# Kernel optimization log

Measured on AMD Instinct MI355X. Metric: run time of the kernel, lower is better.

Reference implementation:

```python
import jax, jax.numpy as jnp
import numpy as np
import math

EMBED_DIM = 768
NUM_HEADS = 12
HEAD_DIM = EMBED_DIM // NUM_HEADS
EPS = 1e-6


def setup_inputs() -> dict:
    key = jax.random.key(0)
    ks = jax.random.split(key, 9)
    T, B, N, D = 4, 4, 1024, EMBED_DIM
    s = 0.02
    return {
        "x": jax.random.normal(ks[0], (T, B, N, D), dtype=jnp.float32),
        "Wq": jax.random.normal(ks[1], (D, D), dtype=jnp.float32) * s,
        "bq": jax.random.normal(ks[2], (D,), dtype=jnp.float32) * s,
        "Wk": jax.random.normal(ks[3], (D, D), dtype=jnp.float32) * s,
        "bk": jax.random.normal(ks[4], (D,), dtype=jnp.float32) * s,
        "Wv": jax.random.normal(ks[5], (D, D), dtype=jnp.float32) * s,
        "bv": jax.random.normal(ks[6], (D,), dtype=jnp.float32) * s,
        "Wo": jax.random.normal(ks[7], (D, D), dtype=jnp.float32) * s,
        "bo": jax.random.normal(ks[8], (D,), dtype=jnp.float32) * s,
    }


def _split_heads(y, T, B, N):
    # [T,B,N,D] -> [T,B,H,N,Dh]
    return y.reshape(T, B, N, NUM_HEADS, HEAD_DIM).transpose(0, 1, 3, 2, 4)


def reference(x, Wq, bq, Wk, bk, Wv, bv, Wo, bo):
    T, B, N, D = x.shape
    # q/k/v projections (nn.Linear: x @ W^T + b)
    q = _split_heads(x @ Wq.T + bq, T, B, N)
    k = _split_heads(x @ Wk.T + bk, T, B, N)
    v = _split_heads(x @ Wv.T + bv, T, B, N)
    # scores = q k^T / sqrt(head_dim)
    scores = jnp.einsum("tbhnd,tbhmd->tbhnm", q, k) / math.sqrt(HEAD_DIM)
    # spike-form normalization: relu then L1-normalize along keys
    act = jax.nn.relu(scores)
    attn = act / (act.sum(axis=-1, keepdims=True) + EPS)
    ctx = jnp.einsum("tbhnm,tbhmd->tbhnd", attn, v)
    # merge heads: [T,B,H,N,Dh] -> [T,B,N,D]
    out = ctx.transpose(0, 1, 3, 2, 4).reshape(T, B, N, D)
    return out @ Wo.T + bo
```

## Files before the change

kernel.cpp:

```cpp
#include <hip/hip_runtime.h>
#include <hip/hip_bf16.h>
#include <cstdint>


typedef __attribute__((ext_vector_type(8))) short short8;
typedef __attribute__((ext_vector_type(4))) float float4v;
typedef __attribute__((ext_vector_type(16))) float float16v;

__device__ __forceinline__ unsigned short f2bf(float f) {
  unsigned int u = __float_as_uint(f);
  u = (u + 0x7fffu + ((u >> 16) & 1u)) >> 16;
  return (unsigned short)u;
}

__device__ __forceinline__ unsigned int pkbf(float a, float b) {
  unsigned int ua = __float_as_uint(a) + 0x8000u;
  unsigned int ub = __float_as_uint(b) + 0x8000u;
  return __builtin_amdgcn_perm(ub, ua, 0x07060302u);
}

__device__ __forceinline__ void gld_lds16(const void* g, void* lds) {
  __builtin_amdgcn_global_load_lds(
      (__attribute__((address_space(1))) void*)(uintptr_t)g,
      (__attribute__((address_space(3))) void*)(uint32_t)(uintptr_t)lds,
      16, 0, 0);
}

__global__ __launch_bounds__(256) void cast4(const float* __restrict__ src,
                                             unsigned short* __restrict__ dst,
                                             int n4) {
  int i = blockIdx.x * 256 + threadIdx.x;
  if (i >= n4) return;
  float4 f = reinterpret_cast<const float4*>(src)[i];
  ushort4 o;
  o.x = f2bf(f.x); o.y = f2bf(f.y); o.z = f2bf(f.z); o.w = f2bf(f.w);
  reinterpret_cast<ushort4*>(dst)[i] = o;
}

template <bool OUT_BF16>
__global__ __launch_bounds__(256) void gemm_bt(
    const unsigned short* __restrict__ A,
    const unsigned short* __restrict__ Bt,
    unsigned short* __restrict__ Cb,
    float* __restrict__ Cf,
    const float* __restrict__ b0, const float* __restrict__ b1,
    const float* __restrict__ b2, int N) {
  constexpr int K = 768;
  __shared__ unsigned short As[128 * 32];
  __shared__ unsigned short Bs[128 * 32];

  const int tid = threadIdx.x;
  const int lane = tid & 63;
  const int w = tid >> 6;
  const int wrow = w >> 1, wcol = w & 1;
  const int l15 = lane & 15, quad = lane >> 4;
  const int i0 = blockIdx.y * 128, j0 = blockIdx.x * 128;

  const unsigned short* ga = A + (size_t)(i0 + 32 * w + (lane >> 2)) * K + (lane & 3) * 8;
  const unsigned short* gb = Bt + (size_t)(j0 + 32 * w + (lane >> 2)) * K + (lane & 3) * 8;

  float4v acc[4][4];
#pragma unroll
  for (int a = 0; a < 4; ++a)
#pragma unroll
    for (int b = 0; b < 4; ++b) acc[a][b] = float4v{0.f, 0.f, 0.f, 0.f};

#pragma unroll 1
  for (int kt = 0; kt < K / 32; ++kt) {
    const unsigned short* pa = ga + kt * 32;
    const unsigned short* pb = gb + kt * 32;
    gld_lds16(pa, &As[(32 * w) * 32]);
    gld_lds16(pa + 16 * K, &As[(32 * w + 16) * 32]);
    gld_lds16(pb, &Bs[(32 * w) * 32]);
    gld_lds16(pb + 16 * K, &Bs[(32 * w + 16) * 32]);
    __syncthreads();

    short8 af[4], bfr[4];
#pragma unroll
    for (int a = 0; a < 4; ++a)
      af[a] = *(const short8*)&As[(wrow * 64 + a * 16 + l15) * 32 + quad * 8];
#pragma unroll
    for (int b = 0; b < 4; ++b)
      bfr[b] = *(const short8*)&Bs[(wcol * 64 + b * 16 + l15) * 32 + quad * 8];
#pragma unroll
    for (int a = 0; a < 4; ++a)
#pragma unroll
      for (int b = 0; b < 4; ++b)
        acc[a][b] = __builtin_amdgcn_mfma_f32_16x16x32_bf16(af[a], bfr[b], acc[a][b], 0, 0, 0);
    __syncthreads();
  }

  const int sel = j0 / 768;
  const float* bp = (sel == 0) ? b0 : ((sel == 1) ? b1 : b2);
#pragma unroll
  for (int a = 0; a < 4; ++a) {
    const int row0 = i0 + wrow * 64 + a * 16 + quad * 4;
#pragma unroll
    for (int b = 0; b < 4; ++b) {
      const int col = j0 + wcol * 64 + b * 16 + l15;
      const float bias = bp[col - sel * 768];
#pragma unroll
      for (int r = 0; r < 4; ++r) {
        const float v = acc[a][b][r] + bias;
        if (OUT_BF16)
          Cb[(size_t)(row0 + r) * N + col] = f2bf(v);
        else
          Cf[(size_t)(row0 + r) * N + col] = v;
      }
    }
  }
}

__global__ __launch_bounds__(256) void transpose_v(
    const unsigned short* __restrict__ qkv, unsigned short* __restrict__ vt) {
  __shared__ unsigned short T[64 * 72];
  const int bz = blockIdx.x;
  const int nt = bz & 15;
  const int tbh = bz >> 4;
  const int tb = tbh / 12, h = tbh % 12;
  const int tid = threadIdx.x;
#pragma unroll
  for (int it = 0; it < 2; ++it) {
    int c = tid + it * 256;
    int row = c >> 3, d0 = (c & 7) * 8;
    const unsigned short* g =
        qkv + (size_t)(tb * 1024 + nt * 64 + row) * 2304 + 1536 + h * 64 + d0;
    *(uint4*)&T[row * 72 + d0] = *(const uint4*)g;
  }
  __syncthreads();
#pragma unroll
  for (int it = 0; it < 2; ++it) {
    int c = tid + it * 256;
    int d = c >> 3, n0 = (c & 7) * 8;
    unsigned short tmp[8];
#pragma unroll
    for (int i = 0; i < 8; ++i) tmp[i] = T[(n0 + i) * 72 + d];
    *(uint4*)&vt[((size_t)(tb * 12 + h) * 64 + d) * 1024 + nt * 64 + n0] =
        *(uint4*)tmp;
  }
}

__global__ __launch_bounds__(256) void attn32(
    const unsigned short* __restrict__ qkv,
    const unsigned short* __restrict__ vt,
    unsigned short* __restrict__ ctx) {
  __shared__ unsigned short Ks[64 * 72];
  __shared__ unsigned short Vs[64 * 72];

  const int tbh = blockIdx.x;
  const int qt = blockIdx.y;
  const int tb = tbh / 12, h = tbh % 12;
  const int tid = threadIdx.x, lane = tid & 63, w = tid >> 6;
  const int l31 = lane & 31, hl = lane >> 5;

  short8 qf[2][4];
#pragma unroll
  for (int qs = 0; qs < 2; ++qs) {
    const unsigned short* qp =
        qkv + (size_t)(tb * 1024 + qt * 256 + w * 64 + qs * 32 + l31) * 2304 +
        h * 64 + hl * 8;
#pragma unroll
    for (int kc = 0; kc < 4; ++kc) qf[qs][kc] = *(const short8*)(qp + kc * 16);
  }

  const int srow = tid >> 3;
  const int sblk = tid & 7;
  const unsigned short* kcol =
      qkv + (size_t)(tb * 1024) * 2304 + 768 + h * 64 + sblk * 8;
  const unsigned short* vcol = vt + ((size_t)tbh * 64 + srow) * 1024 + sblk * 8;
  uint4 kr0, kr1, vr0, vr1;
  auto loadKV = [&](int kv) {
    const unsigned short* kp = kcol + (size_t)(kv * 64 + srow) * 2304;
    kr0 = *(const uint4*)kp;
    kr1 = *(const uint4*)(kp + 32 * 2304);
    const unsigned short* vp = vcol + kv * 64;
    vr0 = *(const uint4*)vp;
    vr1 = *(const uint4*)(vp + 32 * 1024);
  };

  float16v octx[2][2];
#pragma unroll
  for (int qs = 0; qs < 2; ++qs)
#pragma unroll
    for (int dt = 0; dt < 2; ++dt)
#pragma unroll
      for (int i = 0; i < 16; ++i) octx[qs][dt][i] = 0.f;
  float den[2] = {0.f, 0.f};

  loadKV(0);

#pragma unroll 1
  for (int kv = 0; kv < 16; ++kv) {
    __syncthreads();
    *(uint4*)&Ks[srow * 72 + sblk * 8] = kr0;
    *(uint4*)&Ks[(srow + 32) * 72 + sblk * 8] = kr1;
    *(uint4*)&Vs[srow * 72 + sblk * 8] = vr0;
    *(uint4*)&Vs[(srow + 32) * 72 + sblk * 8] = vr1;
    __syncthreads();
    if (kv < 15) loadKV(kv + 1);

#pragma unroll
    for (int qs = 0; qs < 2; ++qs) {
      unsigned int pk[2][8];
#pragma unroll
      for (int mt = 0; mt < 2; ++mt) {
        float16v st;
#pragma unroll
        for (int i = 0; i < 16; ++i) st[i] = 0.f;
#pragma unroll
        for (int kc = 0; kc < 4; ++kc) {
          short8 kf =
              *(const short8*)&Ks[(mt * 32 + l31) * 72 + kc * 16 + hl * 8];
          st = __builtin_amdgcn_mfma_f32_32x32x16_bf16(kf, qf[qs][kc], st, 0, 0, 0);
        }
#pragma unroll
        for (int g = 0; g < 4; ++g) {
          float v0 = st[4 * g + 0]; v0 = v0 > 0.f ? v0 : 0.f;
          float v1 = st[4 * g + 1]; v1 = v1 > 0.f ? v1 : 0.f;
          float v2 = st[4 * g + 2]; v2 = v2 > 0.f ? v2 : 0.f;
          float v3 = st[4 * g + 3]; v3 = v3 > 0.f ? v3 : 0.f;
          den[qs] += (v0 + v1) + (v2 + v3);
          pk[mt][g * 2 + 0] = pkbf(v0, v1);
          pk[mt][g * 2 + 1] = pkbf(v2, v3);
        }
      }
#pragma unroll
      for (int kc = 0; kc < 4; ++kc) {
        const int mt = kc >> 1, gb = (kc & 1) * 2;
        unsigned int a0 = pk[mt][gb * 2 + 0], b0 = pk[mt][gb * 2 + 2];
        unsigned int a1 = pk[mt][gb * 2 + 1], b1 = pk[mt][gb * 2 + 3];
        asm("v_permlane32_swap_b32 %0, %1" : "+v"(a0), "+v"(b0));
        asm("v_permlane32_swap_b32 %0, %1" : "+v"(a1), "+v"(b1));
        union { unsigned int u[4]; short8 s; } pf;
        pf.u[0] = a0; pf.u[1] = a1; pf.u[2] = b0; pf.u[3] = b1;
#pragma unroll
        for (int dt = 0; dt < 2; ++dt) {
          short8 vb =
              *(const short8*)&Vs[(dt * 32 + l31) * 72 + kc * 16 + hl * 8];
          octx[qs][dt] = __builtin_amdgcn_mfma_f32_32x32x16_bf16(
              vb, pf.s, octx[qs][dt], 0, 0, 0);
        }
      }
    }
  }

#pragma unroll
  for (int qs = 0; qs < 2; ++qs) {
    float d = den[qs] + __shfl_xor(den[qs], 32);
    const float sc = 1.f / (d + 8e-6f);
    const size_t qrow = (size_t)(tb * 1024 + qt * 256 + w * 64 + qs * 32 + l31);
#pragma unroll
    for (int dt = 0; dt < 2; ++dt)
#pragma unroll
      for (int g = 0; g < 4; ++g) {
        const float v0 = octx[qs][dt][4 * g + 0] * sc;
        const float v1 = octx[qs][dt][4 * g + 1] * sc;
        const float v2 = octx[qs][dt][4 * g + 2] * sc;
        const float v3 = octx[qs][dt][4 * g + 3] * sc;
        uint2 u;
        u.x = pkbf(v0, v1);
        u.y = pkbf(v2, v3);
        *(uint2*)&ctx[qrow * 768 + h * 64 + dt * 32 + g * 8 + hl * 4] = u;
      }
  }
}

extern "C" void kernel_launch(void* const* d_in, const int* in_sizes, int n_in,
                              void* d_out, int out_size, void* d_ws, size_t ws_size,
                              hipStream_t stream) {
  const float* x  = (const float*)d_in[0];
  const float* Wq = (const float*)d_in[1];
  const float* bq = (const float*)d_in[2];
  const float* Wk = (const float*)d_in[3];
  const float* bk = (const float*)d_in[4];
  const float* Wv = (const float*)d_in[5];
  const float* bv = (const float*)d_in[6];
  const float* Wo = (const float*)d_in[7];
  const float* bo = (const float*)d_in[8];
  float* out = (float*)d_out;

  char* ws = (char*)d_ws;
  unsigned short* XBF  = (unsigned short*)(ws);
  unsigned short* CTX  = (unsigned short*)(ws);
  unsigned short* WQKV = (unsigned short*)(ws + 25165824);
  unsigned short* WOb  = (unsigned short*)(ws + 28704768);
  unsigned short* QKV  = (unsigned short*)(ws + 29884416);
  unsigned short* VT   = (unsigned short*)(ws + 105381888);

  cast4<<<12288, 256, 0, stream>>>(x, XBF, 3145728);
  cast4<<<576, 256, 0, stream>>>(Wq, WQKV, 147456);
  cast4<<<576, 256, 0, stream>>>(Wk, WQKV + 589824, 147456);
  cast4<<<576, 256, 0, stream>>>(Wv, WQKV + 1179648, 147456);
  cast4<<<576, 256, 0, stream>>>(Wo, WOb, 147456);

  gemm_bt<true><<<dim3(18, 128), 256, 0, stream>>>(XBF, WQKV, QKV, nullptr,
                                                   bq, bk, bv, 2304);
  transpose_v<<<3072, 256, 0, stream>>>(QKV, VT);
  attn32<<<dim3(192, 4), 256, 0, stream>>>(QKV, VT, CTX);
  gemm_bt<false><<<dim3(6, 128), 256, 0, stream>>>(CTX, WOb, nullptr, out,
                                                   bo, bo, bo, 768);
}
```

Before: 333.9 us.

## Rewrite GEMMs with register-prefetched 32x32 MFMA tiles and fuse V transpose into QKV GEMM

Replaces the LDS-staged 128x128 GEMM with a 128x256 tile that uses 32x32x16 MFMAs. B fragments are held directly in registers, and the next K-slice of A and B is prefetched in registers while the current one is computed. The QKV GEMM epilogue now writes the V columns straight into the transposed VT layout, so the separate transpose kernel and its global round trip go away. In exchange there is more register pressure, fewer blocks, and B is loaded per wave without LDS sharing. The old unused QKV V-region writes are also skipped for the V section.

```diff
diff --git a/kernel.cpp b/kernel.cpp
--- a/kernel.cpp
+++ b/kernel.cpp
@@ -4,7 +4,6 @@
 
 
 typedef __attribute__((ext_vector_type(8))) short short8;
-typedef __attribute__((ext_vector_type(4))) float float4v;
 typedef __attribute__((ext_vector_type(16))) float float16v;
 
 __device__ __forceinline__ unsigned short f2bf(float f) {
@@ -17,13 +16,6 @@
   unsigned int ua = __float_as_uint(a) + 0x8000u;
   unsigned int ub = __float_as_uint(b) + 0x8000u;
   return __builtin_amdgcn_perm(ub, ua, 0x07060302u);
-}
-
-__device__ __forceinline__ void gld_lds16(const void* g, void* lds) {
-  __builtin_amdgcn_global_load_lds(
-      (__attribute__((address_space(1))) void*)(uintptr_t)g,
-      (__attribute__((address_space(3))) void*)(uint32_t)(uintptr_t)lds,
-      16, 0, 0);
 }
 
 __global__ __launch_bounds__(256) void cast4(const float* __restrict__ src,
@@ -37,106 +29,123 @@
   reinterpret_cast<ushort4*>(dst)[i] = o;
 }
 
-template <bool OUT_BF16>
-__global__ __launch_bounds__(256) void gemm_bt(
+template <bool OUT_BF16, bool FUSE_VT>
+__global__ __launch_bounds__(256) void gemm_rp(
     const unsigned short* __restrict__ A,
     const unsigned short* __restrict__ Bt,
     unsigned short* __restrict__ Cb,
     float* __restrict__ Cf,
+    unsigned short* __restrict__ vtout,
     const float* __restrict__ b0, const float* __restrict__ b1,
     const float* __restrict__ b2, int N) {
   constexpr int K = 768;
-  __shared__ unsigned short As[128 * 32];
-  __shared__ unsigned short Bs[128 * 32];
-
-  const int tid = threadIdx.x;
-  const int lane = tid & 63;
-  const int w = tid >> 6;
-  const int wrow = w >> 1, wcol = w & 1;
-  const int l15 = lane & 15, quad = lane >> 4;
-  const int i0 = blockIdx.y * 128, j0 = blockIdx.x * 128;
-
-  const unsigned short* ga = A + (size_t)(i0 + 32 * w + (lane >> 2)) * K + (lane & 3) * 8;
-  const unsigned short* gb = Bt + (size_t)(j0 + 32 * w + (lane >> 2)) * K + (lane & 3) * 8;
-
-  float4v acc[4][4];
-#pragma unroll
-  for (int a = 0; a < 4; ++a)
-#pragma unroll
-    for (int b = 0; b < 4; ++b) acc[a][b] = float4v{0.f, 0.f, 0.f, 0.f};
+  __shared__ unsigned short As[128 * 36];
+
+  const int tid = threadIdx.x, lane = tid & 63, w = tid >> 6;
+  const int l31 = lane & 31, hl = lane >> 5;
+  const int j0 = blockIdx.x * 256, i0 = blockIdx.y * 128;
+
+  const int ar = tid >> 2, ak = (tid & 3) * 8;
+  const unsigned short* ga = A + (size_t)(i0 + ar) * K + ak;
+  const unsigned short* gb = Bt + (size_t)(j0 + w * 64 + l31) * K + hl * 8;
+
+  float16v acc[4][2];
+#pragma unroll
+  for (int rt = 0; rt < 4; ++rt)
+#pragma unroll
+    for (int ct = 0; ct < 2; ++ct)
+#pragma unroll
+      for (int i = 0; i < 16; ++i) acc[rt][ct][i] = 0.f;
+
+  uint4 a_st[2], a_nx[2], b_st[4], b_nx[4];
+  a_st[0] = *(const uint4*)ga;
+  a_st[1] = *(const uint4*)(ga + 64 * K);
+#pragma unroll
+  for (int ct = 0; ct < 2; ++ct)
+#pragma unroll
+    for (int ks = 0; ks < 2; ++ks)
+      b_st[ct * 2 + ks] = *(const uint4*)(gb + (size_t)ct * 32 * K + ks * 16);
+#pragma unroll
+  for (int i = 0; i < 2; ++i) a_nx[i] = a_st[i];
+#pragma unroll
+  for (int i = 0; i < 4; ++i) b_nx[i] = b_st[i];
 
 #pragma unroll 1
-  for (int kt = 0; kt < K / 32; ++kt) {
-    const unsigned short* pa = ga + kt * 32;
-    const unsigned short* pb = gb + kt * 32;
-    gld_lds16(pa, &As[(32 * w) * 32]);
-    gld_lds16(pa + 16 * K, &As[(32 * w + 16) * 32]);
-    gld_lds16(pb, &Bs[(32 * w) * 32]);
-    gld_lds16(pb + 16 * K, &Bs[(32 * w + 16) * 32]);
+  for (int kt = 0; kt < 24; ++kt) {
     __syncthreads();
-
-    short8 af[4], bfr[4];
-#pragma unroll
-    for (int a = 0; a < 4; ++a)
-      af[a] = *(const short8*)&As[(wrow * 64 + a * 16 + l15) * 32 + quad * 8];
-#pragma unroll
-    for (int b = 0; b < 4; ++b)
-      bfr[b] = *(const short8*)&Bs[(wcol * 64 + b * 16 + l15) * 32 + quad * 8];
-#pragma unroll
-    for (int a = 0; a < 4; ++a)
-#pragma unroll
-      for (int b = 0; b < 4; ++b)
-        acc[a][b] = __builtin_amdgcn_mfma_f32_16x16x32_bf16(af[a], bfr[b], acc[a][b], 0, 0, 0);
+    *(uint4*)&As[ar * 36 + ak] = a_st[0];
+    *(uint4*)&As[(ar + 64) * 36 + ak] = a_st[1];
     __syncthreads();
-  }
-
-  const int sel = j0 / 768;
+    if (kt < 23) {
+      const unsigned short* ga2 = ga + (kt + 1) * 32;
+      a_nx[0] = *(const uint4*)ga2;
+      a_nx[1] = *(const uint4*)(ga2 + 64 * K);
+      const unsigned short* gb2 = gb + (kt + 1) * 32;
+#pragma unroll
+      for (int ct = 0; ct < 2; ++ct)
+#pragma unroll
+        for (int ks = 0; ks < 2; ++ks)
+          b_nx[ct * 2 + ks] =
+              *(const uint4*)(gb2 + (size_t)ct * 32 * K + ks * 16);
+    }
+#pragma unroll
+    for (int ks = 0; ks < 2; ++ks) {
+      short8 af[4];
+#pragma unroll
+      for (int rt = 0; rt < 4; ++rt)
+        af[rt] = *(const short8*)&As[(rt * 32 + l31) * 36 + ks * 16 + hl * 8];
+#pragma unroll
+      for (int rt = 0; rt < 4; ++rt)
+#pragma unroll
+        for (int ct = 0; ct < 2; ++ct) {
+          union { uint4 u; short8 s; } bf;
+          bf.u = b_st[ct * 2 + ks];
+          acc[rt][ct] = __builtin_amdgcn_mfma_f32_32x32x16_bf16(
+              af[rt], bf.s, acc[rt][ct], 0, 0, 0);
+        }
+    }
+#pragma unroll
+    for (int i = 0; i < 2; ++i) a_st[i] = a_nx[i];
+#pragma unroll
+    for (int i = 0; i < 4; ++i) b_st[i] = b_nx[i];
+  }
+
+  const int sel = FUSE_VT ? (blockIdx.x / 3) : 0;
   const float* bp = (sel == 0) ? b0 : ((sel == 1) ? b1 : b2);
 #pragma unroll
-  for (int a = 0; a < 4; ++a) {
-    const int row0 = i0 + wrow * 64 + a * 16 + quad * 4;
-#pragma unroll
-    for (int b = 0; b < 4; ++b) {
-      const int col = j0 + wcol * 64 + b * 16 + l15;
-      const float bias = bp[col - sel * 768];
-#pragma unroll
-      for (int r = 0; r < 4; ++r) {
-        const float v = acc[a][b][r] + bias;
-        if (OUT_BF16)
-          Cb[(size_t)(row0 + r) * N + col] = f2bf(v);
-        else
-          Cf[(size_t)(row0 + r) * N + col] = v;
-      }
+  for (int ct = 0; ct < 2; ++ct) {
+    const int cgl = j0 + w * 64 + ct * 32 + l31;
+    const float bias = bp[cgl - sel * 768];
+    if (FUSE_VT && sel == 2) {
+      const int h = (cgl - 1536) >> 6, d = cgl & 63;
+      const int tb = i0 >> 10, nb = i0 & 1023;
+      unsigned short* vrow = vtout + ((size_t)(tb * 12 + h) * 64 + d) * 1024;
+#pragma unroll
+      for (int rt = 0; rt < 4; ++rt)
+#pragma unroll
+        for (int g = 0; g < 4; ++g) {
+          const float v0 = acc[rt][ct][4 * g + 0] + bias;
+          const float v1 = acc[rt][ct][4 * g + 1] + bias;
+          const float v2 = acc[rt][ct][4 * g + 2] + bias;
+          const float v3 = acc[rt][ct][4 * g + 3] + bias;
+          uint2 u;
+          u.x = pkbf(v0, v1);
+          u.y = pkbf(v2, v3);
+          *(uint2*)&vrow[nb + rt * 32 + g * 8 + hl * 4] = u;
+        }
+    } else {
+#pragma unroll
+      for (int rt = 0; rt < 4; ++rt)
+#pragma unroll
+        for (int reg = 0; reg < 16; ++reg) {
+          const int r = i0 + rt * 32 + (reg & 3) + 8 * (reg >> 2) + 4 * hl;
+          const float v = acc[rt][ct][reg] + bias;
+          if (OUT_BF16)
+            Cb[(size_t)r * N + cgl] = f2bf(v);
+          else
+            Cf[(size_t)r * N + cgl] = v;
+        }
     }
-  }
-}
-
-__global__ __launch_bounds__(256) void transpose_v(
-    const unsigned short* __restrict__ qkv, unsigned short* __restrict__ vt) {
-  __shared__ unsigned short T[64 * 72];
-  const int bz = blockIdx.x;
-  const int nt = bz & 15;
-  const int tbh = bz >> 4;
-  const int tb = tbh / 12, h = tbh % 12;
-  const int tid = threadIdx.x;
-#pragma unroll
-  for (int it = 0; it < 2; ++it) {
-    int c = tid + it * 256;
-    int row = c >> 3, d0 = (c & 7) * 8;
-    const unsigned short* g =
-        qkv + (size_t)(tb * 1024 + nt * 64 + row) * 2304 + 1536 + h * 64 + d0;
-    *(uint4*)&T[row * 72 + d0] = *(const uint4*)g;
-  }
-  __syncthreads();
-#pragma unroll
-  for (int it = 0; it < 2; ++it) {
-    int c = tid + it * 256;
-    int d = c >> 3, n0 = (c & 7) * 8;
-    unsigned short tmp[8];
-#pragma unroll
-    for (int i = 0; i < 8; ++i) tmp[i] = T[(n0 + i) * 72 + d];
-    *(uint4*)&vt[((size_t)(tb * 12 + h) * 64 + d) * 1024 + nt * 64 + n0] =
-        *(uint4*)tmp;
   }
 }
 
@@ -293,10 +302,9 @@
   cast4<<<576, 256, 0, stream>>>(Wv, WQKV + 1179648, 147456);
   cast4<<<576, 256, 0, stream>>>(Wo, WOb, 147456);
 
-  gemm_bt<true><<<dim3(18, 128), 256, 0, stream>>>(XBF, WQKV, QKV, nullptr,
-                                                   bq, bk, bv, 2304);
-  transpose_v<<<3072, 256, 0, stream>>>(QKV, VT);
+  gemm_rp<true, true><<<dim3(9, 128), 256, 0, stream>>>(
+      XBF, WQKV, QKV, nullptr, VT, bq, bk, bv, 2304);
   attn32<<<dim3(192, 4), 256, 0, stream>>>(QKV, VT, CTX);
-  gemm_bt<false><<<dim3(6, 128), 256, 0, stream>>>(CTX, WOb, nullptr, out,
-                                                   bo, bo, bo, 768);
-}
+  gemm_rp<false, false><<<dim3(3, 128), 256, 0, stream>>>(
+      CTX, WOb, nullptr, out, nullptr, bo, bo, bo, 768);
+}
```

Measured after the change: 503.9 us. +50.9%, slower.
